# Kernel optimization log

Measured on AMD Instinct MI355X. Metric: run time of the kernel, lower is better.

## Reference

```python
import jax, jax.numpy as jnp
import numpy as np

N = 100000
E = 1600000
IN_C, HID_C, OUT_C = 128, 256, 40


def sage_conv(x, src, dst, W_l, W_r, b):
    # mean aggregation of source-node features into destination nodes
    msgs = x[src]                                            # [E, d]
    agg = jax.ops.segment_sum(msgs, dst, num_segments=N)     # [N, d]
    deg = jax.ops.segment_sum(jnp.ones((src.shape[0],), x.dtype), dst,
                              num_segments=N)                # [N]
    agg = agg / jnp.clip(deg, 1.0, None)[:, None]
    # out = lin_l(agg) + lin_r(x); weights stored [out, in] like torch
    return agg @ W_l.T + x @ W_r.T + b


def setup_inputs() -> dict:
    key = jax.random.key(0)
    ks = jax.random.split(key, 10)
    s = 0.05
    x = jax.random.normal(ks[0], (N, IN_C), dtype=jnp.float32)
    edge_index = jax.random.randint(ks[1], (2, E), 0, N, dtype=jnp.int64)
    return {
        "x": x,
        "edge_index": edge_index,
        "W_l0": jax.random.normal(ks[2], (HID_C, IN_C), dtype=jnp.float32) * s,
        "W_r0": jax.random.normal(ks[3], (HID_C, IN_C), dtype=jnp.float32) * s,
        "b0": jnp.zeros((HID_C,), jnp.float32),
        "W_l1": jax.random.normal(ks[4], (HID_C, HID_C), dtype=jnp.float32) * s,
        "W_r1": jax.random.normal(ks[5], (HID_C, HID_C), dtype=jnp.float32) * s,
        "b1": jnp.zeros((HID_C,), jnp.float32),
        "W_lo": jax.random.normal(ks[6], (OUT_C, HID_C), dtype=jnp.float32) * s,
        "W_ro": jax.random.normal(ks[7], (OUT_C, HID_C), dtype=jnp.float32) * s,
        "bo": jnp.zeros((OUT_C,), jnp.float32),
    }


def reference(x, edge_index, W_l0, W_r0, b0, W_l1, W_r1, b1, W_lo, W_ro, bo):
    src, dst = edge_index[0], edge_index[1]
    h = jax.nn.relu(sage_conv(x, src, dst, W_l0, W_r0, b0))
    h = jax.nn.relu(sage_conv(h, src, dst, W_l1, W_r1, b1))
    out = sage_conv(h, src, dst, W_lo, W_ro, bo)
    return jax.nn.log_softmax(out, axis=1)
```

## Files before the change

### kernel.cpp

```cpp
#include <hip/hip_runtime.h>
#include <hip/hip_bf16.h>
#include <cstdint>
#include <cstddef>

#define NN   100000
#define NE   1600000
#define HID  256
#define OUTC 40

typedef __attribute__((ext_vector_type(8))) short bf16x8;
typedef __attribute__((ext_vector_type(4))) float f32x4;

static __device__ __forceinline__ ushort f2bf(float f) {
    __hip_bfloat16 h = __float2bfloat16(f);
    return *reinterpret_cast<ushort*>(&h);
}
static __device__ __forceinline__ float bflo(unsigned u) { return __uint_as_float(u << 16); }
static __device__ __forceinline__ float bfhi(unsigned u) { return __uint_as_float(u & 0xffff0000u); }
static __device__ __forceinline__ float ubf(unsigned w, int k) {
    return (float)((w >> (8 * k)) & 255u);
}

__global__ void k_count(const int* __restrict__ dst, int* __restrict__ cnt) {
    int i = blockIdx.x * blockDim.x + threadIdx.x;
    if (i < NE) atomicAdd(&cnt[dst[i]], 1);
}

__global__ void k_blocksum(const int* __restrict__ cnt, int* __restrict__ bsum) {
    __shared__ int s[256];
    int t = threadIdx.x;
    int n = blockIdx.x * 256 + t;
    s[t] = (n < NN) ? cnt[n] : 0;
    __syncthreads();
    for (int off = 128; off; off >>= 1) {
        if (t < off) s[t] += s[t + off];
        __syncthreads();
    }
    if (t == 0) bsum[blockIdx.x] = s[0];
}

__global__ void k_scanblock(const int* __restrict__ bsum, int* __restrict__ boff, int nb) {
    __shared__ int s[512];
    int t = threadIdx.x;
    int v = (t < nb) ? bsum[t] : 0;
    s[t] = v;
    __syncthreads();
    for (int off = 1; off < 512; off <<= 1) {
        int u = (t >= off) ? s[t - off] : 0;
        __syncthreads();
        s[t] += u;
        __syncthreads();
    }
    if (t < nb) boff[t] = s[t] - v;
}

__global__ void k_rowptr(const int* __restrict__ cnt, const int* __restrict__ boff,
                         int* __restrict__ rowptr, int* __restrict__ fillp,
                         float* __restrict__ invd) {
    __shared__ int s[256];
    int t = threadIdx.x;
    int n = blockIdx.x * 256 + t;
    int c = (n < NN) ? cnt[n] : 0;
    s[t] = c;
    __syncthreads();
    for (int off = 1; off < 256; off <<= 1) {
        int u = (t >= off) ? s[t - off] : 0;
        __syncthreads();
        s[t] += u;
        __syncthreads();
    }
    if (n < NN) {
        int excl = boff[blockIdx.x] + s[t] - c;
        rowptr[n] = excl;
        fillp[n]  = excl;
        invd[n]   = 1.0f / (float)(c > 1 ? c : 1);
    }
    if (n == 0) rowptr[NN] = NE;
}

__global__ void k_fill(const int* __restrict__ src, const int* __restrict__ dst,
                       int* __restrict__ fillp, int* __restrict__ colidx) {
    int i = blockIdx.x * blockDim.x + threadIdx.x;
    if (i < NE) {
        int p = atomicAdd(&fillp[dst[i]], 1);
        colidx[p] = src[i];
    }
}

__global__ void k_cvtfrag(const float* __restrict__ W, ushort* __restrict__ dst,
                          int ocreal, int d, int nf) {
    int f = blockIdx.x * 256 + threadIdx.x;
    if (f >= nf) return;
    int lm = f & 15, lk = (f >> 4) & 3;
    int rest = f >> 6;
    int dk = d / 32;
    int kk = rest % dk, cc = rest / dk;
    int row = cc * 16 + lm, col = kk * 32 + lk * 8;
    unsigned q0 = 0, q1 = 0, q2 = 0, q3 = 0;
    if (row < ocreal) {
        const float4* p = (const float4*)(W + (size_t)row * d + col);
        float4 a = p[0], b = p[1];
        q0 = (unsigned)f2bf(a.x) | ((unsigned)f2bf(a.y) << 16);
        q1 = (unsigned)f2bf(a.z) | ((unsigned)f2bf(a.w) << 16);
        q2 = (unsigned)f2bf(b.x) | ((unsigned)f2bf(b.y) << 16);
        q3 = (unsigned)f2bf(b.z) | ((unsigned)f2bf(b.w) << 16);
    }
    *(uint4*)(dst + (size_t)f * 8) = make_uint4(q0, q1, q2, q3);
}

__global__ __launch_bounds__(256) void k_quant_x8(const float* __restrict__ x,
                                                  unsigned char* __restrict__ xq,
                                                  float* __restrict__ sx) {
    int t = threadIdx.x;
    int qw = t >> 4, ql = t & 15;
    int row = blockIdx.x * 16 + qw;
    if (row >= NN) return;
    const float4* p = (const float4*)(x + (size_t)row * 128 + ql * 8);
    float4 a = p[0], b = p[1];
    float v[8] = {a.x, a.y, a.z, a.w, b.x, b.y, b.z, b.w};
    float m = 0.f;
    #pragma unroll
    for (int k = 0; k < 8; ++k) m = fmaxf(m, fabsf(v[k]));
    m = fmaxf(m, __shfl_xor(m, 1));
    m = fmaxf(m, __shfl_xor(m, 2));
    m = fmaxf(m, __shfl_xor(m, 4));
    m = fmaxf(m, __shfl_xor(m, 8));
    float inv = (m > 0.f) ? 127.f / m : 0.f;
    unsigned w0 = 0, w1 = 0;
    #pragma unroll
    for (int k = 0; k < 4; ++k)
        w0 |= ((unsigned)((int)rintf(v[k] * inv) + 128) & 255u) << (8 * k);
    #pragma unroll
    for (int k = 0; k < 4; ++k)
        w1 |= ((unsigned)((int)rintf(v[4 + k] * inv) + 128) & 255u) << (8 * k);
    *(uint2*)(xq + (size_t)row * 128 + ql * 8) = make_uint2(w0, w1);
    if (ql == 0) sx[row] = (m > 0.f) ? m / 127.f : 0.f;
}

__global__ __launch_bounds__(256, 4) void k_layer0(
    const unsigned char* __restrict__ xq, const float* __restrict__ sx,
    const float* __restrict__ xf,
    const ushort* __restrict__ Wl, const ushort* __restrict__ Wr,
    const float* __restrict__ bias, const float* __restrict__ invd,
    const int* __restrict__ rowptr, const int* __restrict__ colidx,
    unsigned char* __restrict__ hq, float* __restrict__ hs)
{
    __shared__ ushort aggS[64 * 128];
    __shared__ int cidxS[2048];
    char* aggSb = (char*)aggS;
    const int t  = threadIdx.x;
    const int r0 = blockIdx.x * 64;
    const int l = t & 63;

    const int ebase = rowptr[r0];
    const int rend  = (r0 + 64 < NN) ? (r0 + 64) : NN;
    const int etot  = rowptr[rend] - ebase;
    const bool inlds = (etot <= 2048);
    if (inlds) {
        for (int i = t; i < etot; i += 256) cidxS[i] = colidx[ebase + i];
    }
    __syncthreads();

    {
        const int gid = t >> 3, li = t & 7;
        const int base = l & ~7;
        for (int rr = gid; rr < 64; rr += 32) {
            const int r = r0 + rr;
            float acc[16];
            #pragma unroll
            for (int k = 0; k < 16; ++k) acc[k] = 0.f;
            float sum_sc = 0.f;
            if (r < NN) {
                const int beg = rowptr[r], end = rowptr[r + 1];
                for (int e = beg; e < end; e += 8) {
                    const int myi = e + li;
                    int se = -1;
                    if (myi < end) se = inlds ? cidxS[myi - ebase] : colidx[myi];
                    float mysc = (se >= 0) ? sx[se] : 0.f;
                    int   sj[8];
                    float sc[8];
                    uint4 u[8];
                    #pragma unroll
                    for (int j = 0; j < 8; ++j) sj[j] = __shfl(se, base + j);
                    #pragma unroll
                    for (int j = 0; j < 8; ++j) sc[j] = __shfl(mysc, base + j);
                    #pragma unroll
                    for (int j = 0; j < 8; ++j) {
                        u[j] = (sj[j] >= 0)
                            ? *(const uint4*)(xq + (((unsigned)sj[j]) << 7) + (li << 4))
                            : make_uint4(0u, 0u, 0u, 0u);
                    }
                    #pragma unroll
                    for (int j = 0; j < 8; ++j) {
                        #pragma unroll
                        for (int wi = 0; wi < 4; ++wi) {
                            unsigned w = (&u[j].x)[wi];
                            acc[wi*4+0] = fmaf(sc[j], ubf(w, 0), acc[wi*4+0]);
                            acc[wi*4+1] = fmaf(sc[j], ubf(w, 1), acc[wi*4+1]);
                            acc[wi*4+2] = fmaf(sc[j], ubf(w, 2), acc[wi*4+2]);
                            acc[wi*4+3] = fmaf(sc[j], ubf(w, 3), acc[wi*4+3]);
                        }
                        sum_sc += sc[j];
                    }
                }
                const float iv = invd[r];
                #pragma unroll
                for (int k = 0; k < 16; ++k) acc[k] = (acc[k] - 128.f * sum_sc) * iv;
            }
            #pragma unroll
            for (int gg = 0; gg < 2; ++gg) {
                unsigned q0 = (unsigned)f2bf(acc[gg*8+0]) | ((unsigned)f2bf(acc[gg*8+1]) << 16);
                unsigned q1 = (unsigned)f2bf(acc[gg*8+2]) | ((unsigned)f2bf(acc[gg*8+3]) << 16);
                unsigned q2 = (unsigned)f2bf(acc[gg*8+4]) | ((unsigned)f2bf(acc[gg*8+5]) << 16);
                unsigned q3 = (unsigned)f2bf(acc[gg*8+6]) | ((unsigned)f2bf(acc[gg*8+7]) << 16);
                int g  = li * 2 + gg;
                int gs = g ^ (rr & 7);
                *(uint4*)(aggSb + (size_t)rr * 256 + (gs << 4)) = make_uint4(q0, q1, q2, q3);
            }
        }
    }
    __syncthreads();

    const int w = t >> 6, lm = l & 15, lk = l >> 4;
    const int rr = w * 16 + lm;
    const int rg = r0 + rr;

    bf16x8 ax[4];
    #pragma unroll
    for (int kk = 0; kk < 4; ++kk) {
        bf16x8 v;
        if (rg < NN) {
            const float4* p = (const float4*)(xf + (size_t)rg * 128 + kk * 32 + lk * 8);
            float4 f0 = p[0], f1 = p[1];
            v[0] = (short)f2bf(f0.x); v[1] = (short)f2bf(f0.y);
            v[2] = (short)f2bf(f0.z); v[3] = (short)f2bf(f0.w);
            v[4] = (short)f2bf(f1.x); v[5] = (short)f2bf(f1.y);
            v[6] = (short)f2bf(f1.z); v[7] = (short)f2bf(f1.w);
        } else v = (bf16x8)(short)0;
        ax[kk] = v;
    }
    bf16x8 agg_reg[4];
    #pragma unroll
    for (int kk = 0; kk < 4; ++kk) {
        int g  = kk * 4 + lk;
        int gs = g ^ (rr & 7);
        agg_reg[kk] = *(const bf16x8*)(aggSb + (size_t)rr * 256 + (gs << 4));
    }

    f32x4 acc[16];
    #pragma unroll
    for (int cc = 0; cc < 16; ++cc) acc[cc] = {0.f, 0.f, 0.f, 0.f};

    #pragma unroll
    for (int kk = 0; kk < 4; ++kk) {
        #pragma unroll
        for (int cc = 0; cc < 16; ++cc) {
            const size_t wf = ((size_t)(cc * 4 + kk) * 64 + l) * 8;
            bf16x8 bl = *(const bf16x8*)(Wl + wf);
            bf16x8 br = *(const bf16x8*)(Wr + wf);
            acc[cc] = __builtin_amdgcn_mfma_f32_16x16x32_bf16(agg_reg[kk], bl, acc[cc], 0, 0, 0);
            acc[cc] = __builtin_amdgcn_mfma_f32_16x16x32_bf16(ax[kk],      br, acc[cc], 0, 0, 0);
        }
    }

    float vmax[4] = {0.f, 0.f, 0.f, 0.f};
    #pragma unroll
    for (int cc = 0; cc < 16; ++cc) {
        const float bv = bias[cc * 16 + lm];
        #pragma unroll
        for (int i = 0; i < 4; ++i) {
            float v = fmaxf(acc[cc][i] + bv, 0.f);
            acc[cc][i] = v;
            vmax[i] = fmaxf(vmax[i], v);
        }
    }
    #pragma unroll
    for (int i = 0; i < 4; ++i) {
        vmax[i] = fmaxf(vmax[i], __shfl_xor(vmax[i], 1));
        vmax[i] = fmaxf(vmax[i], __shfl_xor(vmax[i], 2));
        vmax[i] = fmaxf(vmax[i], __shfl_xor(vmax[i], 4));
        vmax[i] = fmaxf(vmax[i], __shfl_xor(vmax[i], 8));
    }
    float invq[4];
    #pragma unroll
    for (int i = 0; i < 4; ++i) invq[i] = (vmax[i] > 0.f) ? 255.f / vmax[i] : 0.f;
    const int ob = r0 + w * 16 + lk * 4;
    if (lm == 0) {
        #pragma unroll
        for (int i = 0; i < 4; ++i)
            if (ob + i < NN) hs[ob + i] = vmax[i] / 255.f;
    }
    #pragma unroll
    for (int cc = 0; cc < 16; ++cc) {
        #pragma unroll
        for (int i = 0; i < 4; ++i) {
            if (ob + i < NN)
                hq[(size_t)(ob + i) * 256 + cc * 16 + lm] =
                    (unsigned char)(int)rintf(acc[cc][i] * invq[i]);
        }
    }
}

__global__ __launch_bounds__(256, 4) void k_layer1(
    const unsigned char* __restrict__ hq, const float* __restrict__ hs,
    const ushort* __restrict__ Wl, const ushort* __restrict__ Wr,
    const float* __restrict__ bias, const float* __restrict__ invd,
    const int* __restrict__ rowptr, const int* __restrict__ colidx,
    ushort* __restrict__ hout)
{
    __shared__ ushort aggS[64 * 256];
    __shared__ int cidxS[2048];
    char* aggSb = (char*)aggS;
    const int t  = threadIdx.x;
    const int r0 = blockIdx.x * 64;
    const int l = t & 63;

    const int ebase = rowptr[r0];
    const int rend  = (r0 + 64 < NN) ? (r0 + 64) : NN;
    const int etot  = rowptr[rend] - ebase;
    const bool inlds = (etot <= 2048);
    if (inlds) {
        for (int i = t; i < etot; i += 256) cidxS[i] = colidx[ebase + i];
    }
    __syncthreads();

    {
        const int gid = t >> 4, li = t & 15;
        const int base = l & ~15;
        for (int rr = gid; rr < 64; rr += 16) {
            const int r = r0 + rr;
            float acc[16];
            #pragma unroll
            for (int k = 0; k < 16; ++k) acc[k] = 0.f;
            if (r < NN) {
                const int beg = rowptr[r], end = rowptr[r + 1];
                for (int e = beg; e < end; e += 8) {
                    const int myi = e + (li & 7);
                    int se = -1;
                    if (myi < end) se = inlds ? cidxS[myi - ebase] : colidx[myi];
                    float mysc = (se >= 0) ? hs[se] : 0.f;
                    int   sj[8];
                    float sc[8];
                    uint4 u[8];
                    #pragma unroll
                    for (int j = 0; j < 8; ++j) sj[j] = __shfl(se, base + j);
                    #pragma unroll
                    for (int j = 0; j < 8; ++j) sc[j] = __shfl(mysc, base + j);
                    #pragma unroll
                    for (int j = 0; j < 8; ++j) {
                        u[j] = (sj[j] >= 0)
                            ? *(const uint4*)(hq + (((unsigned)sj[j]) << 8) + (li << 4))
                            : make_uint4(0u, 0u, 0u, 0u);
                    }
                    #pragma unroll
                    for (int j = 0; j < 8; ++j) {
                        #pragma unroll
                        for (int wi = 0; wi < 4; ++wi) {
                            unsigned w = (&u[j].x)[wi];
                            acc[wi*4+0] = fmaf(sc[j], ubf(w, 0), acc[wi*4+0]);
                            acc[wi*4+1] = fmaf(sc[j], ubf(w, 1), acc[wi*4+1]);
                            acc[wi*4+2] = fmaf(sc[j], ubf(w, 2), acc[wi*4+2]);
                            acc[wi*4+3] = fmaf(sc[j], ubf(w, 3), acc[wi*4+3]);
                        }
                    }
                }
                const float iv = invd[r];
                #pragma unroll
                for (int k = 0; k < 16; ++k) acc[k] *= iv;
            }
            #pragma unroll
            for (int gg = 0; gg < 2; ++gg) {
                unsigned q0 = (unsigned)f2bf(acc[gg*8+0]) | ((unsigned)f2bf(acc[gg*8+1]) << 16);
                unsigned q1 = (unsigned)f2bf(acc[gg*8+2]) | ((unsigned)f2bf(acc[gg*8+3]) << 16);
                unsigned q2 = (unsigned)f2bf(acc[gg*8+4]) | ((unsigned)f2bf(acc[gg*8+5]) << 16);
                unsigned q3 = (unsigned)f2bf(acc[gg*8+6]) | ((unsigned)f2bf(acc[gg*8+7]) << 16);
                int g  = li * 2 + gg;
                int gs = g ^ (rr & 7);
                *(uint4*)(aggSb + (size_t)rr * 512 + (gs << 4)) = make_uint4(q0, q1, q2, q3);
            }
        }
    }
    __syncthreads();

    const int w = t >> 6, lm = l & 15, lk = l >> 4;
    const int rr = w * 16 + lm;
    const int rg = r0 + rr;

    bf16x8 ax[8];
    {
        const float sr = (rg < NN) ? hs[rg] : 0.f;
        #pragma unroll
        for (int kk = 0; kk < 8; ++kk) {
            uint2 uq = (rg < NN)
                ? *(const uint2*)(hq + (((unsigned)rg) << 8) + kk * 32 + lk * 8)
                : make_uint2(0u, 0u);
            bf16x8 v;
            v[0] = (short)f2bf(sr * ubf(uq.x, 0));
            v[1] = (short)f2bf(sr * ubf(uq.x, 1));
            v[2] = (short)f2bf(sr * ubf(uq.x, 2));
            v[3] = (short)f2bf(sr * ubf(uq.x, 3));
            v[4] = (short)f2bf(sr * ubf(uq.y, 0));
            v[5] = (short)f2bf(sr * ubf(uq.y, 1));
            v[6] = (short)f2bf(sr * ubf(uq.y, 2));
            v[7] = (short)f2bf(sr * ubf(uq.y, 3));
            ax[kk] = v;
        }
    }
    bf16x8 agg_reg[8];
    #pragma unroll
    for (int kk = 0; kk < 8; ++kk) {
        int g  = kk * 4 + lk;
        int gs = g ^ (rr & 7);
        agg_reg[kk] = *(const bf16x8*)(aggSb + (size_t)rr * 512 + (gs << 4));
    }

    for (int cc = 0; cc < 16; ++cc) {
        const int c = cc * 16 + lm;
        f32x4 acc = {0.f, 0.f, 0.f, 0.f};
        #pragma unroll
        for (int kk = 0; kk < 8; ++kk) {
            const size_t wf = ((size_t)(cc * 8 + kk) * 64 + l) * 8;
            bf16x8 bl = *(const bf16x8*)(Wl + wf);
            bf16x8 br = *(const bf16x8*)(Wr + wf);
            acc = __builtin_amdgcn_mfma_f32_16x16x32_bf16(agg_reg[kk], bl, acc, 0, 0, 0);
            acc = __builtin_amdgcn_mfma_f32_16x16x32_bf16(ax[kk],      br, acc, 0, 0, 0);
        }
        const float bv = bias[c];
        #pragma unroll
        for (int i = 0; i < 4; ++i) {
            const int orow = r0 + w * 16 + lk * 4 + i;
            if (orow < NN) {
                float v = fmaxf(acc[i] + bv, 0.f);
                hout[(size_t)orow * HID + c] = f2bf(v);
            }
        }
    }
}

__global__ __launch_bounds__(256, 4) void k_premul(
    const ushort* __restrict__ h1, const ushort* __restrict__ wlo,
    const ushort* __restrict__ wro, const float* __restrict__ bo,
    unsigned char* __restrict__ qq, float* __restrict__ sq, float* __restrict__ rbuf)
{
    const int t = threadIdx.x;
    const int r0 = blockIdx.x * 64;
    const int w = t >> 6, l = t & 63, lm = l & 15, lk = l >> 4;
    const int rr = w * 16 + lm;
    const int rg = r0 + rr;

    f32x4 aq[3], ar[3];
    #pragma unroll
    for (int cc = 0; cc < 3; ++cc) { aq[cc] = {0.f,0.f,0.f,0.f}; ar[cc] = {0.f,0.f,0.f,0.f}; }

    #pragma unroll
    for (int kk = 0; kk < 8; ++kk) {
        bf16x8 a = (rg < NN)
            ? *(const bf16x8*)(h1 + (size_t)rg * 256 + kk * 32 + lk * 8)
            : (bf16x8)(short)0;
        #pragma unroll
        for (int cc = 0; cc < 3; ++cc) {
            const size_t wf = ((size_t)(cc * 8 + kk) * 64 + l) * 8;
            bf16x8 bl = *(const bf16x8*)(wlo + wf);
            bf16x8 br = *(const bf16x8*)(wro + wf);
            aq[cc] = __builtin_amdgcn_mfma_f32_16x16x32_bf16(a, bl, aq[cc], 0, 0, 0);
            ar[cc] = __builtin_amdgcn_mfma_f32_16x16x32_bf16(a, br, ar[cc], 0, 0, 0);
        }
    }

    #pragma unroll
    for (int i = 0; i < 4; ++i) {
        const int orow = r0 + w * 16 + lk * 4 + i;
        if (orow >= NN) continue;
        float m = 0.f;
        #pragma unroll
        for (int cc = 0; cc < 3; ++cc) {
            const int c = cc * 16 + lm;
            if (c < OUTC) m = fmaxf(m, fabsf(aq[cc][i]));
        }
        m = fmaxf(m, __shfl_xor(m, 1));
        m = fmaxf(m, __shfl_xor(m, 2));
        m = fmaxf(m, __shfl_xor(m, 4));
        m = fmaxf(m, __shfl_xor(m, 8));
        const float inv = (m > 0.f) ? 127.f / m : 0.f;
        #pragma unroll
        for (int cc = 0; cc < 3; ++cc) {
            const int c = cc * 16 + lm;
            int code = (c < OUTC) ? (int)rintf(aq[cc][i] * inv) : 0;
            qq[(size_t)orow * 64 + c] = (unsigned char)(code + 128);
            rbuf[(size_t)orow * 64 + c] = (c < OUTC) ? (ar[cc][i] + bo[c]) : 0.f;
        }
        qq[(size_t)orow * 64 + 48 + lm] = (unsigned char)128;
        rbuf[(size_t)orow * 64 + 48 + lm] = 0.f;
        if (lm == 0) sq[orow] = m / 127.f;
    }
}

__global__ __launch_bounds__(256) void k_final(
    const unsigned char* __restrict__ qq, const float* __restrict__ sq,
    const float* __restrict__ rbuf, const float* __restrict__ invd,
    const int* __restrict__ rowptr, const int* __restrict__ colidx,
    float* __restrict__ out)
{
    __shared__ int cidxS[2048];
    const int t = threadIdx.x;
    const int g = t >> 2, li = t & 3;
    const int r0 = blockIdx.x * 64;
    const int row = r0 + g;
    const int l = t & 63;
    const int base = l & ~3;

    const int ebase = rowptr[r0];
    const int rend  = (r0 + 64 < NN) ? (r0 + 64) : NN;
    const int etot  = rowptr[rend] - ebase;
    const bool inlds = (etot <= 2048);
    if (inlds) {
        for (int i = t; i < etot; i += 256) cidxS[i] = colidx[ebase + i];
    }
    __syncthreads();
    if (row >= NN) return;

    float acc[16];
    #pragma unroll
    for (int k = 0; k < 16; ++k) acc[k] = 0.f;
    float sum_sc = 0.f;

    const int beg = rowptr[row], end = rowptr[row + 1];
    for (int e = beg; e < end; e += 8) {
        const int m0 = e + li, m1 = e + 4 + li;
        int se0 = -1, se1 = -1;
        if (m0 < end) se0 = inlds ? cidxS[m0 - ebase] : colidx[m0];
        if (m1 < end) se1 = inlds ? cidxS[m1 - ebase] : colidx[m1];
        float ms0 = (se0 >= 0) ? sq[se0] : 0.f;
        float ms1 = (se1 >= 0) ? sq[se1] : 0.f;
        int   sj[8];
        float sc[8];
        uint4 u[8];
        #pragma unroll
        for (int j = 0; j < 4; ++j) { sj[j] = __shfl(se0, base + j); sc[j] = __shfl(ms0, base + j); }
        #pragma unroll
        for (int j = 4; j < 8; ++j) { sj[j] = __shfl(se1, base + j - 4); sc[j] = __shfl(ms1, base + j - 4); }
        #pragma unroll
        for (int j = 0; j < 8; ++j) {
            u[j] = (sj[j] >= 0)
                ? *(const uint4*)(qq + (((unsigned)sj[j]) << 6) + (li << 4))
                : make_uint4(0u, 0u, 0u, 0u);
        }
        #pragma unroll
        for (int j = 0; j < 8; ++j) {
            #pragma unroll
            for (int wi = 0; wi < 4; ++wi) {
                unsigned w = (&u[j].x)[wi];
                acc[wi*4+0] = fmaf(sc[j], ubf(w, 0), acc[wi*4+0]);
                acc[wi*4+1] = fmaf(sc[j], ubf(w, 1), acc[wi*4+1]);
                acc[wi*4+2] = fmaf(sc[j], ubf(w, 2), acc[wi*4+2]);
                acc[wi*4+3] = fmaf(sc[j], ubf(w, 3), acc[wi*4+3]);
            }
            sum_sc += sc[j];
        }
    }

    const float iv = invd[row];
    const float4* rp = (const float4*)(rbuf + (size_t)row * 64 + li * 16);
    float v[16];
    #pragma unroll
    for (int ch = 0; ch < 4; ++ch) {
        float4 rv = rp[ch];
        v[ch*4+0] = (acc[ch*4+0] - 128.f * sum_sc) * iv + rv.x;
        v[ch*4+1] = (acc[ch*4+1] - 128.f * sum_sc) * iv + rv.y;
        v[ch*4+2] = (acc[ch*4+2] - 128.f * sum_sc) * iv + rv.z;
        v[ch*4+3] = (acc[ch*4+3] - 128.f * sum_sc) * iv + rv.w;
    }
    #pragma unroll
    for (int k = 0; k < 16; ++k)
        if (li * 16 + k >= OUTC) v[k] = -INFINITY;

    float m = v[0];
    #pragma unroll
    for (int k = 1; k < 16; ++k) m = fmaxf(m, v[k]);
    m = fmaxf(m, __shfl_xor(m, 1));
    m = fmaxf(m, __shfl_xor(m, 2));

    float s = 0.f;
    #pragma unroll
    for (int k = 0; k < 16; ++k)
        if (li * 16 + k < OUTC) s += __expf(v[k] - m);
    s += __shfl_xor(s, 1);
    s += __shfl_xor(s, 2);
    const float ls = __logf(s);

    #pragma unroll
    for (int ch = 0; ch < 4; ++ch) {
        const int c = li * 16 + ch * 4;
        if (c < OUTC) {
            float4 o;
            o.x = v[ch*4+0] - m - ls;
            o.y = v[ch*4+1] - m - ls;
            o.z = v[ch*4+2] - m - ls;
            o.w = v[ch*4+3] - m - ls;
            *(float4*)(out + (size_t)row * OUTC + c) = o;
        }
    }
}

extern "C" void kernel_launch(void* const* d_in, const int* in_sizes, int n_in,
                              void* d_out, int out_size, void* d_ws, size_t ws_size,
                              hipStream_t stream) {
    const float* x   = (const float*)d_in[0];
    const int*   ei  = (const int*)d_in[1];
    const int*   src = ei;
    const int*   dst = ei + NE;
    const float* Wl0 = (const float*)d_in[2];
    const float* Wr0 = (const float*)d_in[3];
    const float* b0  = (const float*)d_in[4];
    const float* Wl1 = (const float*)d_in[5];
    const float* Wr1 = (const float*)d_in[6];
    const float* b1  = (const float*)d_in[7];
    const float* Wlo = (const float*)d_in[8];
    const float* Wro = (const float*)d_in[9];
    const float* bo  = (const float*)d_in[10];
    float* out = (float*)d_out;

    char* ws = (char*)d_ws;
    const size_t MB = 1 << 20;
    float*         invd   = (float*)(ws + 0);
    int*           rowptr = (int*)(ws + MB / 2);
    int*           cnt    = (int*)(ws + MB);
    int*           fillp  = (int*)(ws + MB + MB / 2);
    int*           bsum   = (int*)(ws + 2 * MB);
    int*           boff   = (int*)(ws + 2 * MB + MB / 4);
    float*         sx     = (float*)(ws + 2 * MB + MB / 2);
    float*         s0     = (float*)(ws + 3 * MB);
    float*         sq     = (float*)(ws + 3 * MB + MB / 2);
    ushort*        Wb     = (ushort*)(ws + 4 * MB);
    int*           colidx = (int*)(ws + 4 * MB + MB / 2);
    unsigned char* xq8    = (unsigned char*)(ws + 11 * MB);
    unsigned char* qq     = (unsigned char*)(ws + 11 * MB);
    unsigned char* h0q    = (unsigned char*)(ws + 24 * MB);
    float*         rbuf   = (float*)(ws + 24 * MB);
    ushort*        h1     = (ushort*)(ws + 50 * MB);

    ushort* wl0 = Wb;
    ushort* wr0 = Wb + 32768;
    ushort* wl1 = Wb + 65536;
    ushort* wr1 = Wb + 131072;
    ushort* wlo = Wb + 196608;
    ushort* wro = Wb + 208896;

    hipMemsetAsync(cnt, 0, NN * sizeof(int), stream);
    k_count<<<(NE + 255) / 256, 256, 0, stream>>>(dst, cnt);
    const int NB = (NN + 255) / 256;
    k_blocksum<<<NB, 256, 0, stream>>>(cnt, bsum);
    k_scanblock<<<1, 512, 0, stream>>>(bsum, boff, NB);
    k_rowptr<<<NB, 256, 0, stream>>>(cnt, boff, rowptr, fillp, invd);
    k_fill<<<(NE + 255) / 256, 256, 0, stream>>>(src, dst, fillp, colidx);

    k_cvtfrag<<<16, 256, 0, stream>>>(Wl0, wl0, 256, 128, 4096);
    k_cvtfrag<<<16, 256, 0, stream>>>(Wr0, wr0, 256, 128, 4096);
    k_cvtfrag<<<32, 256, 0, stream>>>(Wl1, wl1, 256, 256, 8192);
    k_cvtfrag<<<32, 256, 0, stream>>>(Wr1, wr1, 256, 256, 8192);
    k_cvtfrag<<<6,  256, 0, stream>>>(Wlo, wlo, 40, 256, 1536);
    k_cvtfrag<<<6,  256, 0, stream>>>(Wro, wro, 40, 256, 1536);
    k_quant_x8<<<(NN + 15) / 16, 256, 0, stream>>>(x, xq8, sx);

    const int GB = (NN + 63) / 64;
    k_layer0<<<GB, 256, 0, stream>>>(xq8, sx, x, wl0, wr0, b0, invd, rowptr, colidx, h0q, s0);
    k_layer1<<<GB, 256, 0, stream>>>(h0q, s0, wl1, wr1, b1, invd, rowptr, colidx, h1);
    k_premul<<<GB, 256, 0, stream>>>(h1, wlo, wro, bo, qq, sq, rbuf);
    k_final<<<GB, 256, 0, stream>>>(qq, sq, rbuf, invd, rowptr, colidx, out);
}
```

Measured before the change: 509.5 us.

## Double-buffer neighbor gathers and prestage per-edge scales in LDS

```diff
diff --git a/kernel.cpp b/kernel.cpp
--- a/kernel.cpp
+++ b/kernel.cpp
@@ -137,7 +137,62 @@
     if (ql == 0) sx[row] = (m > 0.f) ? m / 127.f : 0.f;
 }
 
-__global__ __launch_bounds__(256, 4) void k_layer0(
+template<int RSH>
+static __device__ __forceinline__ void ld_batch(
+    const unsigned char* __restrict__ qin,
+    const int* __restrict__ cidxS, const float* __restrict__ scS,
+    const int* __restrict__ colidx, const float* __restrict__ qs, bool inlds,
+    int e, int end, int ebase, int li4,
+    uint4 (&u)[8], float (&sc)[8])
+{
+    #pragma unroll
+    for (int j = 0; j < 8; ++j) {
+        const bool valid = (e + j < end);
+        int sj = 0; float s = 0.f;
+        if (valid) {
+            if (inlds) { sj = cidxS[e + j - ebase]; s = scS[e + j - ebase]; }
+            else       { sj = colidx[e + j];        s = qs[sj]; }
+        }
+        sc[j] = s;
+        u[j] = *(const uint4*)(qin + (((unsigned)sj) << RSH) + li4);
+    }
+}
+
+static __device__ __forceinline__ void acc_batch(
+    const uint4 (&u)[8], const float (&sc)[8], float (&acc)[16], float& sum_sc)
+{
+    #pragma unroll
+    for (int j = 0; j < 8; ++j) {
+        #pragma unroll
+        for (int wi = 0; wi < 4; ++wi) {
+            unsigned w = (&u[j].x)[wi];
+            acc[wi*4+0] = fmaf(sc[j], ubf(w, 0), acc[wi*4+0]);
+            acc[wi*4+1] = fmaf(sc[j], ubf(w, 1), acc[wi*4+1]);
+            acc[wi*4+2] = fmaf(sc[j], ubf(w, 2), acc[wi*4+2]);
+            acc[wi*4+3] = fmaf(sc[j], ubf(w, 3), acc[wi*4+3]);
+        }
+        sum_sc += sc[j];
+    }
+}
+
+static __device__ __forceinline__ void stage_idx_sc(
+    const int* __restrict__ colidx, const float* __restrict__ qs,
+    int ebase, int etot, int t, int* cidxS, float* scS)
+{
+    int myidx[8];
+    #pragma unroll
+    for (int k = 0; k < 8; ++k) {
+        int i = t + k * 256;
+        myidx[k] = (i < etot) ? colidx[ebase + i] : 0;
+    }
+    #pragma unroll
+    for (int k = 0; k < 8; ++k) {
+        int i = t + k * 256;
+        if (i < etot) { cidxS[i] = myidx[k]; scS[i] = qs[myidx[k]]; }
+    }
+}
+
+__global__ __launch_bounds__(256, 3) void k_layer0(
     const unsigned char* __restrict__ xq, const float* __restrict__ sx,
     const float* __restrict__ xf,
     const ushort* __restrict__ Wl, const ushort* __restrict__ Wr,
@@ -147,6 +202,7 @@
 {
     __shared__ ushort aggS[64 * 128];
     __shared__ int cidxS[2048];
+    __shared__ float scS[2048];
     char* aggSb = (char*)aggS;
     const int t  = threadIdx.x;
     const int r0 = blockIdx.x * 64;
@@ -156,14 +212,12 @@
     const int rend  = (r0 + 64 < NN) ? (r0 + 64) : NN;
     const int etot  = rowptr[rend] - ebase;
     const bool inlds = (etot <= 2048);
-    if (inlds) {
-        for (int i = t; i < etot; i += 256) cidxS[i] = colidx[ebase + i];
-    }
+    if (inlds) stage_idx_sc(colidx, sx, ebase, etot, t, cidxS, scS);
     __syncthreads();
 
     {
         const int gid = t >> 3, li = t & 7;
-        const int base = l & ~7;
+        const int li4 = li << 4;
         for (int rr = gid; rr < 64; rr += 32) {
             const int r = r0 + rr;
             float acc[16];
@@ -172,35 +226,18 @@
             float sum_sc = 0.f;
             if (r < NN) {
                 const int beg = rowptr[r], end = rowptr[r + 1];
-                for (int e = beg; e < end; e += 8) {
-                    const int myi = e + li;
-                    int se = -1;
-                    if (myi < end) se = inlds ? cidxS[myi - ebase] : colidx[myi];
-                    float mysc = (se >= 0) ? sx[se] : 0.f;
-                    int   sj[8];
-                    float sc[8];
-                    uint4 u[8];
-                    #pragma unroll
-                    for (int j = 0; j < 8; ++j) sj[j] = __shfl(se, base + j);
-                    #pragma unroll
-                    for (int j = 0; j < 8; ++j) sc[j] = __shfl(mysc, base + j);
-                    #pragma unroll
-                    for (int j = 0; j < 8; ++j) {
-                        u[j] = (sj[j] >= 0)
-                            ? *(const uint4*)(xq + (((unsigned)sj[j]) << 7) + (li << 4))
-                            : make_uint4(0u, 0u, 0u, 0u);
-                    }
-                    #pragma unroll
-                    for (int j = 0; j < 8; ++j) {
-                        #pragma unroll
-                        for (int wi = 0; wi < 4; ++wi) {
-                            unsigned w = (&u[j].x)[wi];
-                            acc[wi*4+0] = fmaf(sc[j], ubf(w, 0), acc[wi*4+0]);
-                            acc[wi*4+1] = fmaf(sc[j], ubf(w, 1), acc[wi*4+1]);
-                            acc[wi*4+2] = fmaf(sc[j], ubf(w, 2), acc[wi*4+2]);
-                            acc[wi*4+3] = fmaf(sc[j], ubf(w, 3), acc[wi*4+3]);
-                        }
-                        sum_sc += sc[j];
+                if (beg < end) {
+                    uint4 uA[8], uB[8];
+                    float scA[8], scB[8];
+                    ld_batch<7>(xq, cidxS, scS, colidx, sx, inlds, beg, end, ebase, li4, uA, scA);
+                    for (int e = beg; e < end; e += 16) {
+                        const bool hasB = (e + 8 < end);
+                        if (hasB)
+                            ld_batch<7>(xq, cidxS, scS, colidx, sx, inlds, e + 8, end, ebase, li4, uB, scB);
+                        acc_batch(uA, scA, acc, sum_sc);
+                        if (e + 16 < end)
+                            ld_batch<7>(xq, cidxS, scS, colidx, sx, inlds, e + 16, end, ebase, li4, uA, scA);
+                        if (hasB) acc_batch(uB, scB, acc, sum_sc);
                     }
                 }
                 const float iv = invd[r];
@@ -301,7 +338,7 @@
     }
 }
 
-__global__ __launch_bounds__(256, 4) void k_layer1(
+__global__ __launch_bounds__(256, 3) void k_layer1(
     const unsigned char* __restrict__ hq, const float* __restrict__ hs,
     const ushort* __restrict__ Wl, const ushort* __restrict__ Wr,
     const float* __restrict__ bias, const float* __restrict__ invd,
@@ -310,6 +347,7 @@
 {
     __shared__ ushort aggS[64 * 256];
     __shared__ int cidxS[2048];
+    __shared__ float scS[2048];
     char* aggSb = (char*)aggS;
     const int t  = threadIdx.x;
     const int r0 = blockIdx.x * 64;
@@ -319,49 +357,32 @@
     const int rend  = (r0 + 64 < NN) ? (r0 + 64) : NN;
     const int etot  = rowptr[rend] - ebase;
     const bool inlds = (etot <= 2048);
-    if (inlds) {
-        for (int i = t; i < etot; i += 256) cidxS[i] = colidx[ebase + i];
-    }
+    if (inlds) stage_idx_sc(colidx, hs, ebase, etot, t, cidxS, scS);
     __syncthreads();
 
     {
         const int gid = t >> 4, li = t & 15;
-        const int base = l & ~15;
+        const int li4 = li << 4;
         for (int rr = gid; rr < 64; rr += 16) {
             const int r = r0 + rr;
             float acc[16];
             #pragma unroll
             for (int k = 0; k < 16; ++k) acc[k] = 0.f;
+            float sum_sc = 0.f;
             if (r < NN) {
                 const int beg = rowptr[r], end = rowptr[r + 1];
-                for (int e = beg; e < end; e += 8) {
-                    const int myi = e + (li & 7);
-                    int se = -1;
-                    if (myi < end) se = inlds ? cidxS[myi - ebase] : colidx[myi];
-                    float mysc = (se >= 0) ? hs[se] : 0.f;
-                    int   sj[8];
-                    float sc[8];
-                    uint4 u[8];
-                    #pragma unroll
-                    for (int j = 0; j < 8; ++j) sj[j] = __shfl(se, base + j);
-                    #pragma unroll
-                    for (int j = 0; j < 8; ++j) sc[j] = __shfl(mysc, base + j);
-                    #pragma unroll
-                    for (int j = 0; j < 8; ++j) {
-                        u[j] = (sj[j] >= 0)
-                            ? *(const uint4*)(hq + (((unsigned)sj[j]) << 8) + (li << 4))
-                            : make_uint4(0u, 0u, 0u, 0u);
-                    }
-                    #pragma unroll
-                    for (int j = 0; j < 8; ++j) {
-                        #pragma unroll
-                        for (int wi = 0; wi < 4; ++wi) {
-                            unsigned w = (&u[j].x)[wi];
-                            acc[wi*4+0] = fmaf(sc[j], ubf(w, 0), acc[wi*4+0]);
-                            acc[wi*4+1] = fmaf(sc[j], ubf(w, 1), acc[wi*4+1]);
-                            acc[wi*4+2] = fmaf(sc[j], ubf(w, 2), acc[wi*4+2]);
-                            acc[wi*4+3] = fmaf(sc[j], ubf(w, 3), acc[wi*4+3]);
-                        }
+                if (beg < end) {
+                    uint4 uA[8], uB[8];
+                    float scA[8], scB[8];
+                    ld_batch<8>(hq, cidxS, scS, colidx, hs, inlds, beg, end, ebase, li4, uA, scA);
+                    for (int e = beg; e < end; e += 16) {
+                        const bool hasB = (e + 8 < end);
+                        if (hasB)
+                            ld_batch<8>(hq, cidxS, scS, colidx, hs, inlds, e + 8, end, ebase, li4, uB, scB);
+                        acc_batch(uA, scA, acc, sum_sc);
+                        if (e + 16 < end)
+                            ld_batch<8>(hq, cidxS, scS, colidx, hs, inlds, e + 16, end, ebase, li4, uA, scA);
+                        if (hasB) acc_batch(uB, scB, acc, sum_sc);
                     }
                 }
                 const float iv = invd[r];
@@ -502,20 +523,18 @@
     float* __restrict__ out)
 {
     __shared__ int cidxS[2048];
+    __shared__ float scS[2048];
     const int t = threadIdx.x;
     const int g = t >> 2, li = t & 3;
+    const int li4 = li << 4;
     const int r0 = blockIdx.x * 64;
     const int row = r0 + g;
-    const int l = t & 63;
-    const int base = l & ~3;
 
     const int ebase = rowptr[r0];
     const int rend  = (r0 + 64 < NN) ? (r0 + 64) : NN;
     const int etot  = rowptr[rend] - ebase;
     const bool inlds = (etot <= 2048);
-    if (inlds) {
-        for (int i = t; i < etot; i += 256) cidxS[i] = colidx[ebase + i];
-    }
+    if (inlds) stage_idx_sc(colidx, sq, ebase, etot, t, cidxS, scS);
     __syncthreads();
     if (row >= NN) return;
 
@@ -525,37 +544,18 @@
     float sum_sc = 0.f;
 
     const int beg = rowptr[row], end = rowptr[row + 1];
-    for (int e = beg; e < end; e += 8) {
-        const int m0 = e + li, m1 = e + 4 + li;
-        int se0 = -1, se1 = -1;
-        if (m0 < end) se0 = inlds ? cidxS[m0 - ebase] : colidx[m0];
-        if (m1 < end) se1 = inlds ? cidxS[m1 - ebase] : colidx[m1];
-        float ms0 = (se0 >= 0) ? sq[se0] : 0.f;
-        float ms1 = (se1 >= 0) ? sq[se1] : 0.f;
-        int   sj[8];
-        float sc[8];
-        uint4 u[8];
-        #pragma unroll
-        for (int j = 0; j < 4; ++j) { sj[j] = __shfl(se0, base + j); sc[j] = __shfl(ms0, base + j); }
-        #pragma unroll
-        for (int j = 4; j < 8; ++j) { sj[j] = __shfl(se1, base + j - 4); sc[j] = __shfl(ms1, base + j - 4); }
-        #pragma unroll
-        for (int j = 0; j < 8; ++j) {
-            u[j] = (sj[j] >= 0)
-                ? *(const uint4*)(qq + (((unsigned)sj[j]) << 6) + (li << 4))
-                : make_uint4(0u, 0u, 0u, 0u);
-        }
-        #pragma unroll
-        for (int j = 0; j < 8; ++j) {
-            #pragma unroll
-            for (int wi = 0; wi < 4; ++wi) {
-                unsigned w = (&u[j].x)[wi];
-                acc[wi*4+0] = fmaf(sc[j], ubf(w, 0), acc[wi*4+0]);
-                acc[wi*4+1] = fmaf(sc[j], ubf(w, 1), acc[wi*4+1]);
-                acc[wi*4+2] = fmaf(sc[j], ubf(w, 2), acc[wi*4+2]);
-                acc[wi*4+3] = fmaf(sc[j], ubf(w, 3), acc[wi*4+3]);
-            }
-            sum_sc += sc[j];
+    if (beg < end) {
+        uint4 uA[8], uB[8];
+        float scA[8], scB[8];
+        ld_batch<6>(qq, cidxS, scS, colidx, sq, inlds, beg, end, ebase, li4, uA, scA);
+        for (int e = beg; e < end; e += 16) {
+            const bool hasB = (e + 8 < end);
+            if (hasB)
+                ld_batch<6>(qq, cidxS, scS, colidx, sq, inlds, e + 8, end, ebase, li4, uB, scB);
+            acc_batch(uA, scA, acc, sum_sc);
+            if (e + 16 < end)
+                ld_batch<6>(qq, cidxS, scS, colidx, sq, inlds, e + 16, end, ebase, li4, uA, scA);
+            if (hasB) acc_batch(uB, scB, acc, sum_sc);
         }
     }
 
```

Result: slower. 626.5 us (+23.0%).
